# Kernel optimization log

Hardware: AMD Instinct MI355X
Metric: run time of the kernel (lower is better)

## Reference

```python
import jax, jax.numpy as jnp
import numpy as np

B, S, HID = 1, 2048, 2048
H, KH, D = 16, 8, 128          # query heads, kv heads, head_dim
GROUPS = H // KH                # num_key_value_groups = 2
EPS = 1e-6
SCALE = D ** -0.5
NEG = -1e9


def rmsnorm(x, w):
    # torch.nn.RMSNorm over last dim with learned weight
    return x * jax.lax.rsqrt(jnp.mean(x * x, axis=-1, keepdims=True) + EPS) * w


def rope(x, cos, sin):
    # x: [b, s, h, d]; cos/sin: [s, d//2]  (rotate-half style, matching apply_rotary_emb_single)
    half = x.shape[-1] // 2
    xr, xi = x[..., :half], x[..., half:]
    c = cos[None, :, None, :]
    s = sin[None, :, None, :]
    return jnp.concatenate([xr * c - xi * s, xr * s + xi * c], axis=-1)


def setup_inputs() -> dict:
    key = jax.random.key(0)
    ks = jax.random.split(key, 8)
    hidden_states = jax.random.normal(ks[0], (B, S, HID), jnp.float32)
    # real RoPE angle tables (theta=1e6, Qwen3-style), shape [S, D//2]
    inv_freq = 1.0 / (1e6 ** (np.arange(0, D, 2, dtype=np.float32) / D))
    ang = np.arange(S, dtype=np.float32)[:, None] * inv_freq[None, :]
    freqs_cos = jnp.asarray(np.cos(ang), jnp.float32)
    freqs_sin = jnp.asarray(np.sin(ang), jnp.float32)
    # additive causal mask [1, S, S]
    causal = jnp.tril(jnp.ones((S, S), jnp.bool_))
    atten_mask = jnp.where(causal, 0.0, NEG).astype(jnp.float32)[None]
    # learned params (no bias: attention_bias=False)
    Wq = jax.random.normal(ks[1], (H * D, HID), jnp.float32) * 0.02
    Wk = jax.random.normal(ks[2], (KH * D, HID), jnp.float32) * 0.02
    Wv = jax.random.normal(ks[3], (KH * D, HID), jnp.float32) * 0.02
    Wo = jax.random.normal(ks[4], (HID, H * D), jnp.float32) * 0.02
    q_norm_w = 1.0 + 0.01 * jax.random.normal(ks[5], (D,), jnp.float32)
    k_norm_w = 1.0 + 0.01 * jax.random.normal(ks[6], (D,), jnp.float32)
    return {"hidden_states": hidden_states, "freqs_cos": freqs_cos, "freqs_sin": freqs_sin,
            "atten_mask": atten_mask, "Wq": Wq, "Wk": Wk, "Wv": Wv, "Wo": Wo,
            "q_norm_w": q_norm_w, "k_norm_w": k_norm_w}


def reference(hidden_states, freqs_cos, freqs_sin, atten_mask, Wq, Wk, Wv, Wo, q_norm_w, k_norm_w):
    b, s, _ = hidden_states.shape
    q = (hidden_states @ Wq.T).reshape(b, s, H, D)
    k = (hidden_states @ Wk.T).reshape(b, s, KH, D)
    v = (hidden_states @ Wv.T).reshape(b, s, KH, D)
    q = rope(rmsnorm(q, q_norm_w), freqs_cos, freqs_sin)
    k = rope(rmsnorm(k, k_norm_w), freqs_cos, freqs_sin)
    # GQA: head i uses kv head i // GROUPS -> repeat kv heads in-order
    k_exp = jnp.repeat(k, GROUPS, axis=2)  # [b, s, H, d]
    v_exp = jnp.repeat(v, GROUPS, axis=2)
    scores = jnp.einsum('bshd,bthd->bhst', q, k_exp) * SCALE + atten_mask[:, None, :, :]
    attn = jax.nn.softmax(scores, axis=-1)
    y = jnp.einsum('bhst,bthd->bshd', attn, v_exp).reshape(b, s, H * D)
    y = y @ Wo.T
    # output_new_cache_only: last-position k (post-norm/RoPE) and raw v per kv head
    k_new = jnp.transpose(k[:, -1], (1, 0, 2))  # [KH, b, D]
    v_new = jnp.transpose(v[:, -1], (1, 0, 2))  # [KH, b, D]
    return y, k_new, v_new
```

## Files before the change

### kernel.cpp

```cpp
#include <hip/hip_runtime.h>
#include <hip/hip_bf16.h>
#include <math.h>

#define S_LEN 2048
#define HID 2048
#define NH 16
#define NKH 8
#define HD 128
#define QKV_N 4096
#define SCALE 0.08838834764831845f
#define EPS 1e-6f
#define LOG2E 1.4426950408889634f
#define QSCALE (SCALE * LOG2E)

typedef __hip_bfloat16 bf16;
typedef unsigned int u32;
typedef __bf16 bf16x8 __attribute__((ext_vector_type(8)));
typedef float f32x4 __attribute__((ext_vector_type(4)));

#define MFMA(a, b, c) __builtin_amdgcn_mfma_f32_16x16x32_bf16(a, b, c, 0, 0, 0)

static __device__ __forceinline__ bf16x8 ld_frag(const bf16* p) {
    return __builtin_bit_cast(bf16x8, *(const uint4*)p);
}

static __device__ __forceinline__ void gload_lds16(const void* g, void* l) {
    __builtin_amdgcn_global_load_lds(
        (const __attribute__((address_space(1))) u32*)g,
        (__attribute__((address_space(3))) u32*)l, 16, 0, 0);
}

__global__ __launch_bounds__(256) void cvt5(
    const float* __restrict__ s0, const float* __restrict__ s1,
    const float* __restrict__ s2, const float* __restrict__ s3,
    const float* __restrict__ s4,
    bf16* __restrict__ d0, bf16* __restrict__ d1, bf16* __restrict__ d2,
    bf16* __restrict__ d3, bf16* __restrict__ d4)
{
    int i = blockIdx.x * 256 + threadIdx.x;
    const float* s; bf16* d; int off;
    if (i < (1 << 20))                   { s = s0; d = d0; off = 0; }
    else if (i < (2 << 20))              { s = s1; d = d1; off = 1 << 20; }
    else if (i < (2 << 20) + (1 << 19))  { s = s2; d = d2; off = 2 << 20; }
    else if (i < (3 << 20))              { s = s3; d = d3; off = (2 << 20) + (1 << 19); }
    else                                 { s = s4; d = d4; off = 3 << 20; }
    int j = i - off;
    float4 v = ((const float4*)s)[j];
    union { ushort4 u; bf16 h[4]; } o;
    o.h[0] = __float2bfloat16(v.x);
    o.h[1] = __float2bfloat16(v.y);
    o.h[2] = __float2bfloat16(v.z);
    o.h[3] = __float2bfloat16(v.w);
    *(ushort4*)(d + 4 * (size_t)j) = o.u;
}

__global__ __launch_bounds__(256, 2) void gemm_qkv(
    const bf16* __restrict__ A, const bf16* __restrict__ B,
    bf16* __restrict__ qkvb, bf16* __restrict__ vT,
    const float* __restrict__ fcos, const float* __restrict__ fsin,
    const float* __restrict__ qw, const float* __restrict__ kw,
    float* __restrict__ knew, float* __restrict__ vnew)
{
    __shared__ bf16 As[2][128 * 64];
    __shared__ bf16 Bs[2][128 * 64];
    __shared__ float red[2][2][64];
    const int tid = threadIdx.x;
    const int n0 = blockIdx.x * 128, m0 = blockIdx.y * 128;
    const int w = tid >> 6, lane = tid & 63;
    const int l15 = lane & 15, quad = lane >> 4;
    const int wr = (w >> 1) * 64;
    const int wcg = (w & 1) * 32;

    f32x4 acc[4][4];
    #pragma unroll
    for (int i = 0; i < 4; ++i)
        #pragma unroll
        for (int j = 0; j < 4; ++j)
            acc[i][j] = f32x4{0.f, 0.f, 0.f, 0.f};

    const int srow8 = lane >> 3;
    const int sls = ((lane & 7) ^ srow8) * 8;

    auto stage = [&](int k0, int nb) {
        #pragma unroll
        for (int j = 0; j < 8; ++j) {
            int c = 8 * w + j;
            if (c < 16) {
                int row = c * 8 + srow8;
                gload_lds16(A + (size_t)(m0 + row) * HID + k0 + sls, &As[nb][c * 512]);
            } else {
                int row = (c - 16) * 8 + srow8;
                gload_lds16(B + (size_t)(n0 + row) * HID + k0 + sls, &Bs[nb][(c - 16) * 512]);
            }
        }
    };

    stage(0, 0);
    for (int kt = 0; kt < HID / 64; ++kt) {
        const int pp = kt & 1;
        __syncthreads();
        if (kt + 1 < HID / 64) stage((kt + 1) * 64, pp ^ 1);

        #pragma unroll
        for (int kc = 0; kc < 2; ++kc) {
            const int ph = ((kc * 4 + quad) ^ (l15 & 7)) * 8;
            bf16x8 av[4], bv[4];
            #pragma unroll
            for (int i = 0; i < 4; ++i)
                av[i] = ld_frag(&As[pp][(wr + i * 16 + l15) * 64 + ph]);
            #pragma unroll
            for (int j = 0; j < 4; ++j)
                bv[j] = ld_frag(&Bs[pp][(wcg + (j & 1) * 16 + (j >> 1) * 64 + l15) * 64 + ph]);
            #pragma unroll
            for (int i = 0; i < 4; ++i)
                #pragma unroll
                for (int j = 0; j < 4; ++j)
                    acc[i][j] = MFMA(av[i], bv[j], acc[i][j]);
        }
    }

    const int hblk = n0 >> 7;
    if (hblk < 24) {
        float ssq[4][4];
        #pragma unroll
        for (int i = 0; i < 4; ++i)
            #pragma unroll
            for (int rr = 0; rr < 4; ++rr) {
                float ss = 0.f;
                #pragma unroll
                for (int j = 0; j < 4; ++j) ss += acc[i][j][rr] * acc[i][j][rr];
                ss += __shfl_xor(ss, 1);
                ss += __shfl_xor(ss, 2);
                ss += __shfl_xor(ss, 4);
                ss += __shfl_xor(ss, 8);
                ssq[i][rr] = ss;
                if (l15 == 0)
                    red[w >> 1][w & 1][i * 16 + quad * 4 + rr] = ss;
            }
        __syncthreads();

        const float* wgt = (hblk < 16) ? qw : kw;
        float wv[4];
        #pragma unroll
        for (int j = 0; j < 4; ++j)
            wv[j] = wgt[wcg + (j & 1) * 16 + (j >> 1) * 64 + l15];
        const size_t cb = (hblk < 16) ? (size_t)hblk * HD
                                      : (size_t)HID + (size_t)(hblk - 16) * HD;

        #pragma unroll
        for (int i = 0; i < 4; ++i)
            #pragma unroll
            for (int rr = 0; rr < 4; ++rr) {
                int rloc = i * 16 + quad * 4 + rr;
                int srow = m0 + wr + rloc;
                float tot = ssq[i][rr] + red[w >> 1][(w & 1) ^ 1][rloc];
                float rrn = rsqrtf(tot * (1.0f / 128.0f) + EPS);
                float x[4], res[4];
                #pragma unroll
                for (int j = 0; j < 4; ++j) x[j] = acc[i][j][rr] * rrn * wv[j];
                #pragma unroll
                for (int j2 = 0; j2 < 2; ++j2) {
                    float c = fcos[srow * 64 + wcg + j2 * 16 + l15];
                    float s = fsin[srow * 64 + wcg + j2 * 16 + l15];
                    res[j2]     = x[j2] * c - x[j2 + 2] * s;
                    res[j2 + 2] = x[j2] * s + x[j2 + 2] * c;
                }
                if (hblk < 16) {
                    #pragma unroll
                    for (int j = 0; j < 4; ++j)
                        qkvb[(size_t)srow * QKV_N + cb + wcg + (j & 1) * 16 +
                             (j >> 1) * 64 + l15] = __float2bfloat16(res[j] * QSCALE);
                } else {
                    #pragma unroll
                    for (int j = 0; j < 4; ++j)
                        qkvb[(size_t)srow * QKV_N + cb + wcg + (j & 1) * 16 +
                             (j >> 1) * 64 + l15] = __float2bfloat16(res[j]);
                    if (srow == S_LEN - 1) {
                        #pragma unroll
                        for (int j = 0; j < 4; ++j)
                            knew[(hblk - 16) * HD + wcg + (j & 1) * 16 +
                                 (j >> 1) * 64 + l15] = res[j];
                    }
                }
            }
    } else {
        const int kh = hblk - 24;
        #pragma unroll
        for (int i = 0; i < 4; ++i) {
            int rowbase = m0 + wr + i * 16 + quad * 4;
            #pragma unroll
            for (int j = 0; j < 4; ++j) {
                int d = wcg + (j & 1) * 16 + (j >> 1) * 64 + l15;
                union { uint2 u; bf16 hh[4]; } pk;
                #pragma unroll
                for (int r = 0; r < 4; ++r)
                    pk.hh[r] = __float2bfloat16(acc[i][j][r]);
                *(uint2*)&vT[(size_t)(kh * HD + d) * S_LEN + rowbase] = pk.u;
                if (rowbase == S_LEN - 4)
                    vnew[kh * HD + d] = acc[i][j][3];
            }
        }
    }
}

__global__ __launch_bounds__(256, 2) void gemm_n64(
    const bf16* __restrict__ A, const bf16* __restrict__ B,
    float* __restrict__ C, int M, int N, int K)
{
    __shared__ bf16 As[2][128 * 64];
    __shared__ bf16 Bs[2][64 * 64];
    const int tid = threadIdx.x;
    const int n0 = blockIdx.x * 64, m0 = blockIdx.y * 128;
    const int w = tid >> 6, lane = tid & 63;
    const int l15 = lane & 15, quad = lane >> 4;

    f32x4 acc[2][4];
    #pragma unroll
    for (int i = 0; i < 2; ++i)
        #pragma unroll
        for (int j = 0; j < 4; ++j)
            acc[i][j] = f32x4{0.f, 0.f, 0.f, 0.f};

    const int srow8 = lane >> 3;
    const int sls = ((lane & 7) ^ srow8) * 8;

    auto stage = [&](int k0, int nb) {
        #pragma unroll
        for (int j = 0; j < 6; ++j) {
            int c = 6 * w + j;
            if (c < 16) {
                int row = c * 8 + srow8;
                gload_lds16(A + (size_t)(m0 + row) * K + k0 + sls, &As[nb][c * 512]);
            } else {
                int row = (c - 16) * 8 + srow8;
                gload_lds16(B + (size_t)(n0 + row) * K + k0 + sls, &Bs[nb][(c - 16) * 512]);
            }
        }
    };

    stage(0, 0);
    for (int kt = 0; kt < K / 64; ++kt) {
        const int pp = kt & 1;
        __syncthreads();
        if (kt + 1 < K / 64) stage((kt + 1) * 64, pp ^ 1);

        #pragma unroll
        for (int kc = 0; kc < 2; ++kc) {
            const int ph = ((kc * 4 + quad) ^ (l15 & 7)) * 8;
            bf16x8 av[2], bv[4];
            av[0] = ld_frag(&As[pp][(w * 32 + l15) * 64 + ph]);
            av[1] = ld_frag(&As[pp][(w * 32 + 16 + l15) * 64 + ph]);
            #pragma unroll
            for (int j = 0; j < 4; ++j)
                bv[j] = ld_frag(&Bs[pp][(j * 16 + l15) * 64 + ph]);
            #pragma unroll
            for (int i = 0; i < 2; ++i)
                #pragma unroll
                for (int j = 0; j < 4; ++j)
                    acc[i][j] = MFMA(av[i], bv[j], acc[i][j]);
        }
    }

    #pragma unroll
    for (int i = 0; i < 2; ++i)
        #pragma unroll
        for (int j = 0; j < 4; ++j)
            #pragma unroll
            for (int r = 0; r < 4; ++r)
                C[(size_t)(m0 + w * 32 + i * 16 + quad * 4 + r) * N +
                  n0 + j * 16 + l15] = acc[i][j][r];
}

__global__ __launch_bounds__(256, 2) void attn_mfma(
    const bf16* __restrict__ qkvb, const bf16* __restrict__ vT,
    bf16* __restrict__ outb)
{
    __shared__ bf16 Ks[2][64 * 128];
    __shared__ bf16 Vs[2][128 * 64];
    __shared__ bf16 Ps[4][16 * 72];
    __shared__ float lred[4][16];

    const int x = blockIdx.x;
    const int h = blockIdx.y, kvh = h >> 1;
    int a = (x & 1) ? (31 - (x >> 1)) : (x >> 1);
    const int qb = (h < 8) ? a : 31 - a;
    const int tid = threadIdx.x, w = tid >> 6, lane = tid & 63;
    const int l15 = lane & 15, quad = lane >> 4;
    const int qw0 = qb * 64 + w * 16;

    bf16x8 qf[4];
    #pragma unroll
    for (int dk = 0; dk < 4; ++dk)
        qf[dk] = ld_frag(qkvb + (size_t)(qw0 + l15) * QKV_N +
                         h * HD + dk * 32 + quad * 8);

    f32x4 o[8];
    #pragma unroll
    for (int dt = 0; dt < 8; ++dt) o[dt] = f32x4{0.f, 0.f, 0.f, 0.f};
    float l_st = 0.f;

    auto stage = [&](int t, int nb) {
        const int kt0 = t * 64;
        if (w < 2) {
            #pragma unroll
            for (int c = 0; c < 8; ++c) {
                int chunk = w * 8 + c;
                int row = 4 * chunk + (lane >> 4);
                int ls = (lane & 15) ^ (row & 15);
                gload_lds16(qkvb + (size_t)(kt0 + row) * QKV_N + HID +
                            kvh * HD + ls * 8,
                            &Ks[nb][chunk * 512]);
            }
        } else {
            #pragma unroll
            for (int c = 0; c < 8; ++c) {
                int chunk = (w - 2) * 8 + c;
                int row = 8 * chunk + (lane >> 3);
                int ls = (lane & 7) ^ ((lane >> 3) & 7);
                gload_lds16(vT + (size_t)(kvh * HD + row) * S_LEN + kt0 + ls * 8,
                            &Vs[nb][chunk * 512]);
            }
        }
    };

    stage(0, 0);
    for (int t = 0; t <= qb; ++t) {
        const int pp = t & 1;
        const int kt0 = t * 64;
        __syncthreads();
        if (t < qb) stage(t + 1, pp ^ 1);

        f32x4 sc[4];
        #pragma unroll
        for (int mt = 0; mt < 4; ++mt) sc[mt] = f32x4{0.f, 0.f, 0.f, 0.f};
        #pragma unroll
        for (int dk = 0; dk < 4; ++dk)
            #pragma unroll
            for (int mt = 0; mt < 4; ++mt) {
                bf16x8 kf = ld_frag(&Ks[pp][(mt * 16 + l15) * 128 +
                                            (((dk * 4 + quad) ^ l15) & 15) * 8]);
                sc[mt] = MFMA(kf, qf[dk], sc[mt]);
            }

        if (kt0 + 63 > qw0) {
            #pragma unroll
            for (int mt = 0; mt < 4; ++mt)
                #pragma unroll
                for (int r = 0; r < 4; ++r) {
                    int kg = kt0 + mt * 16 + quad * 4 + r;
                    if (kg > qw0 + l15) sc[mt][r] = -1e30f;
                }
        }

        #pragma unroll
        for (int mt = 0; mt < 4; ++mt) {
            union { uint2 u; bf16 hh[4]; } pk;
            #pragma unroll
            for (int r = 0; r < 4; ++r) {
                float p = exp2f(sc[mt][r]);
                pk.hh[r] = __float2bfloat16(p);
                l_st += p;
            }
            *(uint2*)&Ps[w][l15 * 72 + mt * 16 + quad * 4] = pk.u;
        }

        asm volatile("s_waitcnt lgkmcnt(0)" ::: "memory");
        __builtin_amdgcn_s_barrier();

        #pragma unroll
        for (int kc = 0; kc < 2; ++kc) {
            bf16x8 pf[4];
            #pragma unroll
            for (int j = 0; j < 4; ++j)
                pf[j] = ld_frag(&Ps[j][l15 * 72 + kc * 32 + quad * 8]);
            #pragma unroll
            for (int dt = 0; dt < 2; ++dt) {
                bf16x8 vf = ld_frag(&Vs[pp][((w * 2 + dt) * 16 + l15) * 64 +
                                            (((kc * 4 + quad) ^ (l15 & 7)) * 8)]);
                #pragma unroll
                for (int j = 0; j < 4; ++j)
                    o[dt * 4 + j] = MFMA(vf, pf[j], o[dt * 4 + j]);
            }
        }
    }

    l_st += __shfl_xor(l_st, 16, 64);
    l_st += __shfl_xor(l_st, 32, 64);
    if (lane < 16) lred[w][lane] = l_st;
    __syncthreads();
    #pragma unroll
    for (int j = 0; j < 4; ++j) {
        float inv = 1.0f / lred[j][l15];
        int qg = qb * 64 + j * 16 + l15;
        #pragma unroll
        for (int dt = 0; dt < 2; ++dt) {
            union { uint2 u; bf16 hh[4]; } pk;
            #pragma unroll
            for (int r = 0; r < 4; ++r)
                pk.hh[r] = __float2bfloat16(o[dt * 4 + j][r] * inv);
            *(uint2*)&outb[(size_t)qg * HID + h * HD + w * 32 + dt * 16 + quad * 4] = pk.u;
        }
    }
}

extern "C" void kernel_launch(void* const* d_in, const int* in_sizes, int n_in,
                              void* d_out, int out_size, void* d_ws, size_t ws_size,
                              hipStream_t stream) {
    const float* hidden = (const float*)d_in[0];
    const float* fcos   = (const float*)d_in[1];
    const float* fsin   = (const float*)d_in[2];
    const float* Wq = (const float*)d_in[4];
    const float* Wk = (const float*)d_in[5];
    const float* Wv = (const float*)d_in[6];
    const float* Wo = (const float*)d_in[7];
    const float* qw = (const float*)d_in[8];
    const float* kw = (const float*)d_in[9];
    float* out = (float*)d_out;

    bf16* qkvb  = (bf16*)d_ws;
    bf16* vT    = qkvb + (size_t)S_LEN * QKV_N;
    bf16* attnb = vT + (size_t)NKH * HD * S_LEN;
    bf16* wqkvb = attnb + (size_t)S_LEN * HID;
    bf16* hidb  = wqkvb + (size_t)QKV_N * HID;
    bf16* wob   = hidb + (size_t)S_LEN * HID;

    float* knew = out + (size_t)S_LEN * HID;
    float* vnew = knew + NKH * HD;

    cvt5<<<16384, 256, 0, stream>>>(
        hidden, Wq, Wk, Wv, Wo,
        hidb, wqkvb, wqkvb + (size_t)HID * HID,
        wqkvb + (size_t)(HID + NKH * HD) * HID, wob);

    gemm_qkv<<<dim3(QKV_N / 128, S_LEN / 128), 256, 0, stream>>>(
        hidb, wqkvb, qkvb, vT, fcos, fsin, qw, kw, knew, vnew);

    attn_mfma<<<dim3(32, NH), 256, 0, stream>>>(qkvb, vT, attnb);

    gemm_n64<<<dim3(HID / 64, S_LEN / 128), 256, 0, stream>>>(
        attnb, wob, out, S_LEN, HID, HID);
}
```

Baseline: 240.5 us.

## Split QK^T work by key rows per wave instead of query rows

Each wave now computes scores for all 64 query rows against its own 16-key slice, keeping all four query fragment sets in registers and loading one K fragment per dk step instead of four. This cuts LDS reads of K per wave by four and lets the causal mask apply only on the diagonal tile. Row sums are now partial per wave and reduced across waves through shared memory at the end. In exchange it uses more registers for the query fragments (16 bf16x8 per lane), which may pressure occupancy under the two-blocks-per-CU launch bound.

```diff
diff --git a/kernel.cpp b/kernel.cpp
--- a/kernel.cpp
+++ b/kernel.cpp
@@ -278,7 +278,7 @@
     __shared__ bf16 Ks[2][64 * 128];
     __shared__ bf16 Vs[2][128 * 64];
     __shared__ bf16 Ps[4][16 * 72];
-    __shared__ float lred[4][16];
+    __shared__ float lred[4][4][16];
 
     const int x = blockIdx.x;
     const int h = blockIdx.y, kvh = h >> 1;
@@ -286,18 +286,19 @@
     const int qb = (h < 8) ? a : 31 - a;
     const int tid = threadIdx.x, w = tid >> 6, lane = tid & 63;
     const int l15 = lane & 15, quad = lane >> 4;
-    const int qw0 = qb * 64 + w * 16;
-
-    bf16x8 qf[4];
-    #pragma unroll
-    for (int dk = 0; dk < 4; ++dk)
-        qf[dk] = ld_frag(qkvb + (size_t)(qw0 + l15) * QKV_N +
-                         h * HD + dk * 32 + quad * 8);
+
+    bf16x8 qf[4][4];
+    #pragma unroll
+    for (int j = 0; j < 4; ++j)
+        #pragma unroll
+        for (int dk = 0; dk < 4; ++dk)
+            qf[j][dk] = ld_frag(qkvb + (size_t)(qb * 64 + j * 16 + l15) * QKV_N +
+                                h * HD + dk * 32 + quad * 8);
 
     f32x4 o[8];
     #pragma unroll
     for (int dt = 0; dt < 8; ++dt) o[dt] = f32x4{0.f, 0.f, 0.f, 0.f};
-    float l_st = 0.f;
+    float l_st[4] = {0.f, 0.f, 0.f, 0.f};
 
     auto stage = [&](int t, int nb) {
         const int kt0 = t * 64;
@@ -326,42 +327,39 @@
     stage(0, 0);
     for (int t = 0; t <= qb; ++t) {
         const int pp = t & 1;
-        const int kt0 = t * 64;
         __syncthreads();
         if (t < qb) stage(t + 1, pp ^ 1);
 
         f32x4 sc[4];
         #pragma unroll
-        for (int mt = 0; mt < 4; ++mt) sc[mt] = f32x4{0.f, 0.f, 0.f, 0.f};
-        #pragma unroll
-        for (int dk = 0; dk < 4; ++dk)
-            #pragma unroll
-            for (int mt = 0; mt < 4; ++mt) {
-                bf16x8 kf = ld_frag(&Ks[pp][(mt * 16 + l15) * 128 +
-                                            (((dk * 4 + quad) ^ l15) & 15) * 8]);
-                sc[mt] = MFMA(kf, qf[dk], sc[mt]);
-            }
-
-        if (kt0 + 63 > qw0) {
-            #pragma unroll
-            for (int mt = 0; mt < 4; ++mt)
-                #pragma unroll
-                for (int r = 0; r < 4; ++r) {
-                    int kg = kt0 + mt * 16 + quad * 4 + r;
-                    if (kg > qw0 + l15) sc[mt][r] = -1e30f;
-                }
-        }
-
-        #pragma unroll
-        for (int mt = 0; mt < 4; ++mt) {
+        for (int j = 0; j < 4; ++j) sc[j] = f32x4{0.f, 0.f, 0.f, 0.f};
+        #pragma unroll
+        for (int dk = 0; dk < 4; ++dk) {
+            bf16x8 kf = ld_frag(&Ks[pp][(w * 16 + l15) * 128 +
+                                        (((dk * 4 + quad) ^ l15) & 15) * 8]);
+            #pragma unroll
+            for (int j = 0; j < 4; ++j)
+                sc[j] = MFMA(kf, qf[j][dk], sc[j]);
+        }
+
+        if (t == qb) {
+            #pragma unroll
+            for (int j = 0; j < 4; ++j)
+                #pragma unroll
+                for (int r = 0; r < 4; ++r)
+                    if (w * 16 + quad * 4 + r > j * 16 + l15) sc[j][r] = -1e30f;
+        }
+
+        #pragma unroll
+        for (int j = 0; j < 4; ++j) {
             union { uint2 u; bf16 hh[4]; } pk;
             #pragma unroll
             for (int r = 0; r < 4; ++r) {
-                float p = exp2f(sc[mt][r]);
+                float p = exp2f(sc[j][r]);
                 pk.hh[r] = __float2bfloat16(p);
-                l_st += p;
-            }
-            *(uint2*)&Ps[w][l15 * 72 + mt * 16 + quad * 4] = pk.u;
+                l_st[j] += p;
+            }
+            *(uint2*)&Ps[j][l15 * 72 + w * 16 + quad * 4] = pk.u;
         }
 
         asm volatile("s_waitcnt lgkmcnt(0)" ::: "memory");
@@ -384,13 +382,20 @@
         }
     }
 
-    l_st += __shfl_xor(l_st, 16, 64);
-    l_st += __shfl_xor(l_st, 32, 64);
-    if (lane < 16) lred[w][lane] = l_st;
+    #pragma unroll
+    for (int j = 0; j < 4; ++j) {
+        l_st[j] += __shfl_xor(l_st[j], 16, 64);
+        l_st[j] += __shfl_xor(l_st[j], 32, 64);
+    }
+    if (lane < 16) {
+        #pragma unroll
+        for (int j = 0; j < 4; ++j) lred[w][j][lane] = l_st[j];
+    }
     __syncthreads();
     #pragma unroll
     for (int j = 0; j < 4; ++j) {
-        float inv = 1.0f / lred[j][l15];
+        float inv = 1.0f / (lred[0][j][l15] + lred[1][j][l15] +
+                            lred[2][j][l15] + lred[3][j][l15]);
         int qg = qb * 64 + j * 16 + l15;
         #pragma unroll
         for (int dt = 0; dt < 2; ++dt) {
```

New measurement: 240.6 us. Within noise of the previous version (+0.0%).
